# Performance work log

Measured on AMD Instinct MI355X. Metric: run time of the kernel, lower is better.

The kernel has to match this reference:

```python
import jax, jax.numpy as jnp
import numpy as np

B, L, P, V, D = 8, 2048, 576, 32000, 2560
IGNORE_INDEX = -100
T = L - 1 + P  # image token removed, P patch embeddings spliced in


def setup_inputs() -> dict:
    key = jax.random.key(0)
    k1, k2, k3, k4, k5 = jax.random.split(key, 5)
    input_ids = jax.random.randint(k1, (B, L), 0, V, dtype=jnp.int32)
    # exactly one image-token position per sample (avoid first/last slot)
    img_pos = jax.random.randint(k2, (B,), 1, L - 2, dtype=jnp.int32)
    labels = jax.random.randint(k3, (B, L), 0, V, dtype=jnp.int32)
    embed_table = jax.random.normal(k4, (V, D), dtype=jnp.float32) * 0.02
    image_features = jax.random.normal(k5, (B, P, D), dtype=jnp.float32)
    return dict(embed_table=embed_table, image_features=image_features,
                input_ids=input_ids, labels=labels, img_pos=img_pos)


def reference(embed_table, image_features, input_ids, labels, img_pos):
    # Fused version of the per-sample splice loop:
    # out[b] = concat(embed(ids[b, :pos]), image_features[b], embed(ids[b, pos+1:]))
    tok_emb = embed_table[input_ids]                      # [B, L, D]
    j = jnp.arange(T, dtype=jnp.int32)[None, :]           # [1, T]
    pos = img_pos[:, None]                                # [B, 1]
    is_img = (j >= pos) & (j < pos + P)                   # [B, T]
    # token source index: before image -> j; after image -> skip img token
    tok_idx = jnp.clip(jnp.where(j < pos, j, j - P + 1), 0, L - 1)  # [B, T]
    img_idx = jnp.clip(j - pos, 0, P - 1)                 # [B, T]
    emb_tok = jnp.take_along_axis(tok_emb, tok_idx[..., None], axis=1)        # [B,T,D]
    emb_img = jnp.take_along_axis(image_features, img_idx[..., None], axis=1)  # [B,T,D]
    new_input_embeds = jnp.where(is_img[..., None], emb_img, emb_tok)
    lab_tok = jnp.take_along_axis(labels, tok_idx, axis=1)
    new_labels = jnp.where(is_img, jnp.int32(IGNORE_INDEX), lab_tok)
    attention_mask = jnp.ones((B, T), dtype=bool)
    position_ids = jnp.broadcast_to(jnp.arange(T, dtype=jnp.int32), (B, T))
    return new_input_embeds, new_labels, attention_mask, position_ids
```

## Files before the change

### kernel.cpp

```cpp
#include <hip/hip_runtime.h>

#define Bn 8
#define Ln 2048
#define Pn 576
#define Vn 32000
#define Dn 2560
#define Tn (Ln - 1 + Pn)
#define IGNORE_INDEX (-100)

__global__ __launch_bounds__(640) void splice_kernel(
    const float* __restrict__ embed_table,
    const float* __restrict__ image_features,
    const int*   __restrict__ input_ids,
    const int*   __restrict__ labels,
    const int*   __restrict__ img_pos,
    float* __restrict__ out)
{
    const int t = blockIdx.x;
    const int b = blockIdx.y;
    const int pos = img_pos[b];

    const bool is_img = (t >= pos) && (t < pos + Pn);

    const float4* __restrict__ src;
    int tok_idx = 0;
    if (is_img) {
        const int img_idx = t - pos;
        src = (const float4*)(image_features + ((size_t)b * Pn + img_idx) * Dn);
    } else {
        tok_idx = (t < pos) ? t : (t - Pn + 1);
        tok_idx = min(max(tok_idx, 0), Ln - 1);
        const int id = input_ids[b * Ln + tok_idx];
        src = (const float4*)(embed_table + (size_t)id * Dn);
    }

    float4* __restrict__ dst = (float4*)(out + ((size_t)b * Tn + t) * Dn);
    dst[threadIdx.x] = src[threadIdx.x];

    if (threadIdx.x == 0) {
        const size_t nBT  = (size_t)Bn * Tn;
        const size_t base = nBT * Dn;
        const size_t idx  = (size_t)b * Tn + t;
        float lab;
        if (is_img) {
            lab = (float)IGNORE_INDEX;
        } else {
            lab = (float)labels[b * Ln + tok_idx];
        }
        out[base + idx]            = lab;
        out[base + nBT + idx]      = 1.0f;
        out[base + 2 * nBT + idx]  = (float)t;
    }
}

extern "C" void kernel_launch(void* const* d_in, const int* in_sizes, int n_in,
                              void* d_out, int out_size, void* d_ws, size_t ws_size,
                              hipStream_t stream) {
    const float* embed_table    = (const float*)d_in[0];
    const float* image_features = (const float*)d_in[1];
    const int*   input_ids      = (const int*)d_in[2];
    const int*   labels         = (const int*)d_in[3];
    const int*   img_pos        = (const int*)d_in[4];
    float* out = (float*)d_out;

    dim3 grid(Tn, Bn);
    dim3 block(640);
    splice_kernel<<<grid, block, 0, stream>>>(embed_table, image_features,
                                              input_ids, labels, img_pos, out);
}
```

Before: 486.6 us.

## Use persistent grid-stride blocks with software-pipelined row prefetch

Replaces the one-block-per-row launch with a fixed grid of 192x8 blocks of 320 threads. Each block walks rows with a stride and loads the next row's two float4 chunks into registers before storing the current row. This is meant to cut per-block launch and scheduling overhead and to keep more loads in flight per thread. In exchange there are fewer resident waves, a persistent loop, and more registers per thread.

```diff
diff --git a/kernel.cpp b/kernel.cpp
--- a/kernel.cpp
+++ b/kernel.cpp
@@ -7,8 +7,10 @@
 #define Dn 2560
 #define Tn (Ln - 1 + Pn)
 #define IGNORE_INDEX (-100)
+#define BLK 320
+#define GRIDX 192
 
-__global__ __launch_bounds__(640) void splice_kernel(
+__global__ __launch_bounds__(BLK) void splice_kernel(
     const float* __restrict__ embed_table,
     const float* __restrict__ image_features,
     const int*   __restrict__ input_ids,
@@ -16,40 +18,60 @@
     const int*   __restrict__ img_pos,
     float* __restrict__ out)
 {
-    const int t = blockIdx.x;
-    const int b = blockIdx.y;
+    const int b   = blockIdx.y;
+    const int tid = threadIdx.x;
     const int pos = img_pos[b];
 
-    const bool is_img = (t >= pos) && (t < pos + Pn);
+    const int* __restrict__ ids_row = input_ids + b * Ln;
+    const int* __restrict__ lab_row = labels    + b * Ln;
 
-    const float4* __restrict__ src;
-    int tok_idx = 0;
-    if (is_img) {
-        const int img_idx = t - pos;
-        src = (const float4*)(image_features + ((size_t)b * Pn + img_idx) * Dn);
-    } else {
-        tok_idx = (t < pos) ? t : (t - Pn + 1);
-        tok_idx = min(max(tok_idx, 0), Ln - 1);
-        const int id = input_ids[b * Ln + tok_idx];
-        src = (const float4*)(embed_table + (size_t)id * Dn);
-    }
+    const size_t nBT  = (size_t)Bn * Tn;
+    float* __restrict__ outL = out + nBT * (size_t)Dn;
+    float* __restrict__ outM = outL + nBT;
+    float* __restrict__ outP = outM + nBT;
 
-    float4* __restrict__ dst = (float4*)(out + ((size_t)b * Tn + t) * Dn);
-    dst[threadIdx.x] = src[threadIdx.x];
+    auto src_of = [&](int t, int& lab) -> const float4* {
+        if (t >= pos && t < pos + Pn) {
+            lab = IGNORE_INDEX;
+            return (const float4*)(image_features +
+                                   ((size_t)b * Pn + (t - pos)) * Dn);
+        }
+        int tok = (t < pos) ? t : (t - Pn + 1);
+        tok = min(max(tok, 0), Ln - 1);
+        lab = lab_row[tok];
+        const int id = ids_row[tok];
+        return (const float4*)(embed_table + (size_t)id * Dn);
+    };
 
-    if (threadIdx.x == 0) {
-        const size_t nBT  = (size_t)Bn * Tn;
-        const size_t base = nBT * Dn;
-        const size_t idx  = (size_t)b * Tn + t;
-        float lab;
-        if (is_img) {
-            lab = (float)IGNORE_INDEX;
-        } else {
-            lab = (float)labels[b * Ln + tok_idx];
+    int t = blockIdx.x;
+    int lab_c;
+    const float4* src_c = src_of(t, lab_c);
+    float4 a0 = src_c[tid];
+    float4 a1 = src_c[tid + BLK];
+
+    while (t < Tn) {
+        const int tn = t + GRIDX;
+
+        int lab_n = 0;
+        const float4* src_n = src_c;
+        if (tn < Tn) src_n = src_of(tn, lab_n);
+        float4 b0 = src_n[tid];
+        float4 b1 = src_n[tid + BLK];
+
+        float4* __restrict__ dst =
+            (float4*)(out + ((size_t)b * Tn + t) * Dn);
+        dst[tid]       = a0;
+        dst[tid + BLK] = a1;
+
+        if (tid == 0) {
+            const size_t idx = (size_t)b * Tn + t;
+            outL[idx] = (float)lab_c;
+            outM[idx] = 1.0f;
+            outP[idx] = (float)t;
         }
-        out[base + idx]            = lab;
-        out[base + nBT + idx]      = 1.0f;
-        out[base + 2 * nBT + idx]  = (float)t;
+
+        a0 = b0; a1 = b1; lab_c = lab_n; src_c = src_n;
+        t = tn;
     }
 }
 
@@ -63,8 +85,8 @@
     const int*   img_pos        = (const int*)d_in[4];
     float* out = (float*)d_out;
 
-    dim3 grid(Tn, Bn);
-    dim3 block(640);
+    dim3 grid(GRIDX, Bn);
+    dim3 block(BLK);
     splice_kernel<<<grid, block, 0, stream>>>(embed_table, image_features,
                                               input_ids, labels, img_pos, out);
 }
```

New measurement: 497.2 us. +2.2%, slower.
